# Kernel tuning notes

Measured on AMD Instinct MI355X. Metric: run time of the kernel, lower is better.

The kernel has to match this reference:

```python
import jax, jax.numpy as jnp
import numpy as np

B, T, D, H = 2, 2048, 512, 8
HD = D // H  # head_dim = 64


def setup_inputs() -> dict:
    key = jax.random.key(0)
    k1, k2, k3, k4 = jax.random.split(key, 4)
    scale = 1.0 / np.sqrt(D)
    x = jax.random.normal(k1, (B, T, D), dtype=jnp.float32)
    periods = jax.random.randint(k2, (B, H), 0, 64, dtype=jnp.int32)
    w_qkv = jax.random.normal(k3, (3 * D, D), dtype=jnp.float32) * scale
    b_qkv = jnp.zeros((3 * D,), dtype=jnp.float32)
    w_out = jax.random.normal(k4, (D, D), dtype=jnp.float32) * scale
    b_out = jnp.zeros((D,), dtype=jnp.float32)
    return {"x": x, "periods": periods, "w_qkv": w_qkv, "b_qkv": b_qkv,
            "w_out": w_out, "b_out": b_out}


def reference(x, periods, w_qkv, b_qkv, w_out, b_out):
    # qkv projection: (B,T,3D) -> (3,B,H,T,HD)
    qkv = x @ w_qkv.T + b_qkv
    qkv = qkv.reshape(B, T, 3, H, HD).transpose(2, 0, 3, 1, 4)
    q, k, v = qkv[0], qkv[1], qkv[2]

    # periodic-causal mask: valid iff j <= i and (i-j) % p == 0, p = max(period,1)
    i_idx = jnp.arange(T, dtype=jnp.int32)[:, None]   # (T,1)
    j_idx = jnp.arange(T, dtype=jnp.int32)[None, :]   # (1,T)
    diff = i_idx - j_idx                              # (T,T)
    p = jnp.maximum(periods, 1)[:, :, None, None]     # (B,H,1,1)
    valid = (diff >= 0) & ((diff % p) == 0)           # (B,H,T,T)

    scores = jnp.einsum('bhqd,bhkd->bhqk', q, k) / np.sqrt(HD)
    scores = jnp.where(valid, scores, jnp.finfo(scores.dtype).min)
    attn = jax.nn.softmax(scores, axis=-1)

    out = jnp.einsum('bhqk,bhkd->bhqd', attn, v)
    out = out.transpose(0, 2, 1, 3).reshape(B, T, D)
    return out @ w_out.T + b_out
```

## Files before the change

kernel.cpp:

```cpp
#include <hip/hip_runtime.h>
#include <math.h>

#define B_  2
#define T_  2048
#define D_  512
#define H_  8
#define HD_ 64
#define QKVS (3*D_)

typedef __bf16 bf16x8 __attribute__((ext_vector_type(8)));
typedef float  f32x4  __attribute__((ext_vector_type(4)));

__device__ inline unsigned short f2bf(float f) {
  unsigned int u = __float_as_uint(f);
  return (unsigned short)((u + 0x7FFFu + ((u >> 16) & 1u)) >> 16);
}
__device__ inline unsigned int pack2bf(float lo, float hi) {
  return (unsigned int)f2bf(lo) | ((unsigned int)f2bf(hi) << 16);
}

__global__ void cast_f32_bf16(const float* __restrict__ src,
                              unsigned short* __restrict__ dst, int n4) {
  int i = blockIdx.x * blockDim.x + threadIdx.x;
  if (i < n4) {
    float4 v = ((const float4*)src)[i];
    ushort4 o;
    o.x = f2bf(v.x); o.y = f2bf(v.y); o.z = f2bf(v.z); o.w = f2bf(v.w);
    ((ushort4*)dst)[i] = o;
  }
}

template<int BF16OUT>
__global__ __launch_bounds__(256)
void gemm_nt_mfma(const unsigned short* __restrict__ A,
                  const unsigned short* __restrict__ Bw,
                  const float* __restrict__ bias, void* __restrict__ Cv,
                  int M, int N, int K) {
  __shared__ short Asd[128 * 32];
  __shared__ short Bsd[64 * 32];

  const int tid = threadIdx.x;
  const int w   = tid >> 6;
  const int l   = tid & 63;
  const int wr  = w >> 1;
  const int wc  = w & 1;
  const int q   = l >> 4;
  const int ml  = l & 15;
  const int arow = l >> 2;
  const int kch  = (l & 3) * 8;

  const int rowbase = blockIdx.y * 128;
  const int colbase = blockIdx.x * 64;

  f32x4 acc[4][2] = {};

  for (int k0 = 0; k0 < K; k0 += 32) {
    __syncthreads();
    #pragma unroll
    for (int s = 0; s < 2; ++s) {
      const unsigned short* g =
          A + (size_t)(rowbase + s * 64 + w * 16 + arow) * K + k0 + kch;
      short* lp = &Asd[s * 2048 + w * 512];
      __builtin_amdgcn_global_load_lds(
          (const __attribute__((address_space(1))) void*)g,
          (__attribute__((address_space(3))) void*)lp, 16, 0, 0);
    }
    {
      const unsigned short* g =
          Bw + (size_t)(colbase + w * 16 + arow) * K + k0 + kch;
      short* lp = &Bsd[w * 512];
      __builtin_amdgcn_global_load_lds(
          (const __attribute__((address_space(1))) void*)g,
          (__attribute__((address_space(3))) void*)lp, 16, 0, 0);
    }
    __syncthreads();

    bf16x8 af[4], bfr[2];
    #pragma unroll
    for (int mi = 0; mi < 4; ++mi)
      af[mi] = *(const bf16x8*)&Asd[(wr * 64 + mi * 16 + ml) * 32 + q * 8];
    #pragma unroll
    for (int ni = 0; ni < 2; ++ni)
      bfr[ni] = *(const bf16x8*)&Bsd[(wc * 32 + ni * 16 + ml) * 32 + q * 8];
    #pragma unroll
    for (int mi = 0; mi < 4; ++mi)
      #pragma unroll
      for (int ni = 0; ni < 2; ++ni)
        acc[mi][ni] = __builtin_amdgcn_mfma_f32_16x16x32_bf16(
            af[mi], bfr[ni], acc[mi][ni], 0, 0, 0);
  }

  #pragma unroll
  for (int mi = 0; mi < 4; ++mi) {
    #pragma unroll
    for (int ni = 0; ni < 2; ++ni) {
      const int col = colbase + wc * 32 + ni * 16 + ml;
      const float bv = bias[col];
      #pragma unroll
      for (int r = 0; r < 4; ++r) {
        const int row = rowbase + wr * 64 + mi * 16 + q * 4 + r;
        const float val = acc[mi][ni][r] + bv;
        if (BF16OUT)
          ((unsigned short*)Cv)[(size_t)row * N + col] = f2bf(val);
        else
          ((float*)Cv)[(size_t)row * N + col] = val;
      }
    }
  }
}

template<int BF16OUT>
__global__ __launch_bounds__(256)
void gemm_nt_mfma128(const unsigned short* __restrict__ A,
                     const unsigned short* __restrict__ Bw,
                     const float* __restrict__ bias, void* __restrict__ Cv,
                     int M, int N, int K) {
  __shared__ short Asd[128 * 32];
  __shared__ short Bsd[128 * 32];

  const int tid = threadIdx.x;
  const int w   = tid >> 6;
  const int l   = tid & 63;
  const int wr  = w >> 1;
  const int wc  = w & 1;
  const int q   = l >> 4;
  const int ml  = l & 15;
  const int arow = l >> 2;
  const int kch  = (l & 3) * 8;

  const int rowbase = blockIdx.y * 128;
  const int colbase = blockIdx.x * 128;

  f32x4 acc[4][4] = {};

  for (int k0 = 0; k0 < K; k0 += 32) {
    __syncthreads();
    #pragma unroll
    for (int s = 0; s < 2; ++s) {
      const unsigned short* ga =
          A + (size_t)(rowbase + s * 64 + w * 16 + arow) * K + k0 + kch;
      __builtin_amdgcn_global_load_lds(
          (const __attribute__((address_space(1))) void*)ga,
          (__attribute__((address_space(3))) void*)&Asd[s * 2048 + w * 512],
          16, 0, 0);
      const unsigned short* gb =
          Bw + (size_t)(colbase + s * 64 + w * 16 + arow) * K + k0 + kch;
      __builtin_amdgcn_global_load_lds(
          (const __attribute__((address_space(1))) void*)gb,
          (__attribute__((address_space(3))) void*)&Bsd[s * 2048 + w * 512],
          16, 0, 0);
    }
    __syncthreads();

    bf16x8 af[4], bfr[4];
    #pragma unroll
    for (int mi = 0; mi < 4; ++mi)
      af[mi] = *(const bf16x8*)&Asd[(wr * 64 + mi * 16 + ml) * 32 + q * 8];
    #pragma unroll
    for (int ni = 0; ni < 4; ++ni)
      bfr[ni] = *(const bf16x8*)&Bsd[(wc * 64 + ni * 16 + ml) * 32 + q * 8];
    #pragma unroll
    for (int mi = 0; mi < 4; ++mi)
      #pragma unroll
      for (int ni = 0; ni < 4; ++ni)
        acc[mi][ni] = __builtin_amdgcn_mfma_f32_16x16x32_bf16(
            af[mi], bfr[ni], acc[mi][ni], 0, 0, 0);
  }

  #pragma unroll
  for (int mi = 0; mi < 4; ++mi) {
    #pragma unroll
    for (int ni = 0; ni < 4; ++ni) {
      const int col = colbase + wc * 64 + ni * 16 + ml;
      const float bv = bias[col];
      #pragma unroll
      for (int r = 0; r < 4; ++r) {
        const int row = rowbase + wr * 64 + mi * 16 + q * 4 + r;
        const float val = acc[mi][ni][r] + bv;
        if (BF16OUT)
          ((unsigned short*)Cv)[(size_t)row * N + col] = f2bf(val);
        else
          ((float*)Cv)[(size_t)row * N + col] = val;
      }
    }
  }
}

__global__ __launch_bounds__(64)
void attn_flash(const unsigned short* __restrict__ qkv,
                const int* __restrict__ periods,
                unsigned short* __restrict__ ao) {
  const int bh = blockIdx.x, slot = blockIdx.y;
  int p = periods[bh]; if (p < 1) p = 1;
  const int qt = slot / p;
  const int r  = slot - qt * p;
  const int L  = (T_ - 1 - r) / p + 1;
  if (qt >= ((L + 15) >> 4)) return;
  const int b = bh >> 3, h = bh & 7;
  const int q0 = qt << 4;
  const int nq = min(16, L - q0);
  const int Nk = min(L, q0 + 16);

  const int lane = threadIdx.x;
  const int Q = lane >> 4, c = lane & 15;

  __shared__ unsigned short Qs[16 * 72];
  __shared__ unsigned short Ks[32 * 72];
  __shared__ unsigned short Vs[32 * 70];

  const size_t rowb = (size_t)b * T_ * QKVS + (size_t)h * HD_;

  {
    const int u = lane >> 2, ch3 = lane & 3;
    const int t = q0 + min(u, nq - 1);
    const unsigned short* g = qkv + rowb + (size_t)(r + t * p) * QKVS + ch3 * 16;
    int4 v0 = ((const int4*)g)[0];
    int4 v1 = ((const int4*)g)[1];
    *(int4*)&Qs[u * 72 + ch3 * 16 + 0] = v0;
    *(int4*)&Qs[u * 72 + ch3 * 16 + 8] = v1;
  }
  __syncthreads();
  bf16x8 qf[2];
  qf[0] = *(const bf16x8*)&Qs[c * 72 + Q * 8];
  qf[1] = *(const bf16x8*)&Qs[c * 72 + Q * 8 + 32];

  float m_run = -3.0e38f, l_run = 0.f;
  f32x4 o[4] = {};
  const size_t kb = rowb + D_;
  const size_t vb = rowb + 2 * D_;
  const int kap = lane >> 1, ke = lane & 1;

  for (int k0 = 0; k0 < Nk; k0 += 32) {
    {
      const int t = min(k0 + kap, Nk - 1);
      const unsigned short* gk = qkv + kb + (size_t)(r + t * p) * QKVS + ke * 32;
      const unsigned short* gv = qkv + vb + (size_t)(r + t * p) * QKVS + ke * 32;
      int4 a0 = ((const int4*)gk)[0], a1 = ((const int4*)gk)[1],
           a2 = ((const int4*)gk)[2], a3 = ((const int4*)gk)[3];
      int4 b0 = ((const int4*)gv)[0], b1 = ((const int4*)gv)[1],
           b2 = ((const int4*)gv)[2], b3 = ((const int4*)gv)[3];
      __syncthreads();
      *(int4*)&Ks[kap * 72 + ke * 32 + 0]  = a0;
      *(int4*)&Ks[kap * 72 + ke * 32 + 8]  = a1;
      *(int4*)&Ks[kap * 72 + ke * 32 + 16] = a2;
      *(int4*)&Ks[kap * 72 + ke * 32 + 24] = a3;
      unsigned int* vw = (unsigned int*)Vs + kap * 35 + ke * 16;
      int4 bb[4] = {b0, b1, b2, b3};
      #pragma unroll
      for (int i = 0; i < 4; ++i) {
        vw[i * 4 + 0] = bb[i].x; vw[i * 4 + 1] = bb[i].y;
        vw[i * 4 + 2] = bb[i].z; vw[i * 4 + 3] = bb[i].w;
      }
      __syncthreads();
    }

    f32x4 s[2];
    #pragma unroll
    for (int mt = 0; mt < 2; ++mt) {
      bf16x8 a0 = *(const bf16x8*)&Ks[(mt * 16 + c) * 72 + Q * 8];
      bf16x8 a1 = *(const bf16x8*)&Ks[(mt * 16 + c) * 72 + Q * 8 + 32];
      f32x4 acc = {};
      acc = __builtin_amdgcn_mfma_f32_16x16x32_bf16(a0, qf[0], acc, 0, 0, 0);
      acc = __builtin_amdgcn_mfma_f32_16x16x32_bf16(a1, qf[1], acc, 0, 0, 0);
      s[mt] = acc;
    }

    float pvv[8];
    float tmax = -3.0e38f;
    #pragma unroll
    for (int mt = 0; mt < 2; ++mt)
      #pragma unroll
      for (int rg = 0; rg < 4; ++rg) {
        const int kk = k0 + mt * 16 + Q * 4 + rg;
        float v = s[mt][rg] * 0.125f;
        v = (kk <= q0 + c) ? v : -3.0e38f;
        pvv[mt * 4 + rg] = v;
        tmax = fmaxf(tmax, v);
      }
    tmax = fmaxf(tmax, __shfl_xor(tmax, 16));
    tmax = fmaxf(tmax, __shfl_xor(tmax, 32));
    const float m_new = fmaxf(m_run, tmax);
    const float alpha = __expf(m_run - m_new);
    float tsum = 0.f;
    #pragma unroll
    for (int i = 0; i < 8; ++i) { pvv[i] = __expf(pvv[i] - m_new); tsum += pvv[i]; }
    tsum += __shfl_xor(tsum, 16);
    tsum += __shfl_xor(tsum, 32);
    l_run = l_run * alpha + tsum;
    m_run = m_new;

    unsigned int pk0[2], pk1[2];
    pk0[0] = pack2bf(pvv[0], pvv[1]); pk0[1] = pack2bf(pvv[2], pvv[3]);
    pk1[0] = pack2bf(pvv[4], pvv[5]); pk1[1] = pack2bf(pvv[6], pvv[7]);
    int dw[4];
    const int sq2 = (Q & 1) << 1;
    #pragma unroll
    for (int d = 0; d < 4; ++d) {
      const int src = ((sq2 + (d >> 1)) << 4) + c;
      const int v0 = __shfl((int)pk0[d & 1], src);
      const int v1 = __shfl((int)pk1[d & 1], src);
      dw[d] = (Q >= 2) ? v1 : v0;
    }
    int4 bi = make_int4(dw[0], dw[1], dw[2], dw[3]);
    bf16x8 pb = *(bf16x8*)&bi;

    #pragma unroll
    for (int ch = 0; ch < 4; ++ch) {
      unsigned short vh[8];
      #pragma unroll
      for (int j = 0; j < 8; ++j)
        vh[j] = Vs[(Q * 8 + j) * 70 + ch * 16 + c];
      unsigned int vi[4];
      #pragma unroll
      for (int j = 0; j < 4; ++j)
        vi[j] = (unsigned int)vh[2 * j] | ((unsigned int)vh[2 * j + 1] << 16);
      int4 ai4 = make_int4((int)vi[0], (int)vi[1], (int)vi[2], (int)vi[3]);
      bf16x8 af = *(bf16x8*)&ai4;
      f32x4 oo = o[ch];
      #pragma unroll
      for (int t2 = 0; t2 < 4; ++t2) oo[t2] *= alpha;
      o[ch] = __builtin_amdgcn_mfma_f32_16x16x32_bf16(af, pb, oo, 0, 0, 0);
    }
  }

  if (c < nq) {
    const float invl = 1.f / l_run;
    const int gq = r + (q0 + c) * p;
    unsigned int* dst =
        (unsigned int*)(ao + (size_t)(b * T_ + gq) * D_ + h * HD_);
    #pragma unroll
    for (int ch = 0; ch < 4; ++ch)
      #pragma unroll
      for (int rp = 0; rp < 2; ++rp) {
        const int dhalf = ch * 16 + Q * 4 + rp * 2;
        dst[dhalf >> 1] =
            pack2bf(o[ch][rp * 2] * invl, o[ch][rp * 2 + 1] * invl);
      }
  }
}

extern "C" void kernel_launch(void* const* d_in, const int* in_sizes, int n_in,
                              void* d_out, int out_size, void* d_ws, size_t ws_size,
                              hipStream_t stream) {
  const float* x      = (const float*)d_in[0];
  const int*   period = (const int*)  d_in[1];
  const float* w_qkv  = (const float*)d_in[2];
  const float* b_qkv  = (const float*)d_in[3];
  const float* w_out  = (const float*)d_in[4];
  const float* b_out  = (const float*)d_in[5];
  float* out = (float*)d_out;

  const int M = B_ * T_;

  char* ws = (char*)d_ws;
  unsigned short* xb   = (unsigned short*)(ws);
  unsigned short* wqb  = (unsigned short*)(ws + (size_t)M * D_ * 2);
  unsigned short* wob  = (unsigned short*)(ws + (size_t)M * D_ * 2
                                              + (size_t)QKVS * D_ * 2);
  unsigned short* qkvb = (unsigned short*)(ws + (size_t)M * D_ * 2
                                              + (size_t)QKVS * D_ * 2
                                              + (size_t)D_ * D_ * 2);
  unsigned short* aob  = xb;

  cast_f32_bf16<<<dim3((M * D_ / 4 + 255) / 256), dim3(256), 0, stream>>>(
      x, xb, M * D_ / 4);
  cast_f32_bf16<<<dim3((QKVS * D_ / 4 + 255) / 256), dim3(256), 0, stream>>>(
      w_qkv, wqb, QKVS * D_ / 4);
  cast_f32_bf16<<<dim3((D_ * D_ / 4 + 255) / 256), dim3(256), 0, stream>>>(
      w_out, wob, D_ * D_ / 4);

  gemm_nt_mfma128<1><<<dim3(QKVS / 128, M / 128), dim3(256), 0, stream>>>(
      xb, wqb, b_qkv, qkvb, M, QKVS, D_);

  attn_flash<<<dim3(16, 192), dim3(64), 0, stream>>>(qkvb, period, aob);

  gemm_nt_mfma<0><<<dim3(D_ / 64, M / 128), dim3(256), 0, stream>>>(
      aob, wob, b_out, out, M, D_, D_);
}
```

Before: 125.6 us.

## Share K/V tiles across four waves in attention and fuse cast kernels

The attention kernel now uses 256-thread blocks of four waves. Each wave owns 16 queries of a 64-query group, and all four share one K tile and one transposed V tile in LDS. V is stored transposed, so the PV MFMA operand becomes a single vector LDS read instead of eight scalar gathers plus packing. Waves skip key tiles beyond their causal range, which reduces global K/V traffic per query and shrinks the grid from 192 to 63 slots. The three f32-to-bf16 cast launches are merged into one kernel to save launch overhead, at the cost of idle waves and barrier stalls for the early-query waves in each group.

```diff
diff --git a/kernel.cpp b/kernel.cpp
--- a/kernel.cpp
+++ b/kernel.cpp
@@ -19,15 +19,25 @@
   return (unsigned int)f2bf(lo) | ((unsigned int)f2bf(hi) << 16);
 }
 
-__global__ void cast_f32_bf16(const float* __restrict__ src,
-                              unsigned short* __restrict__ dst, int n4) {
+__global__ void cast_all(const float* __restrict__ x,
+                         const float* __restrict__ wq,
+                         const float* __restrict__ wo,
+                         unsigned short* __restrict__ xb,
+                         unsigned short* __restrict__ wqb,
+                         unsigned short* __restrict__ wob) {
+  const int n_x  = (B_ * T_ * D_) / 4;
+  const int n_wq = (QKVS * D_) / 4;
+  const int n_wo = (D_ * D_) / 4;
   int i = blockIdx.x * blockDim.x + threadIdx.x;
-  if (i < n4) {
-    float4 v = ((const float4*)src)[i];
-    ushort4 o;
-    o.x = f2bf(v.x); o.y = f2bf(v.y); o.z = f2bf(v.z); o.w = f2bf(v.w);
-    ((ushort4*)dst)[i] = o;
-  }
+  const float* src; unsigned short* dst; int off;
+  if (i < n_x)                { src = x;  dst = xb;  off = i; }
+  else if (i < n_x + n_wq)    { src = wq; dst = wqb; off = i - n_x; }
+  else if (i < n_x + n_wq + n_wo) { src = wo; dst = wob; off = i - n_x - n_wq; }
+  else return;
+  float4 v = ((const float4*)src)[off];
+  ushort4 o;
+  o.x = f2bf(v.x); o.y = f2bf(v.y); o.z = f2bf(v.z); o.w = f2bf(v.w);
+  ((ushort4*)dst)[off] = o;
 }
 
 template<int BF16OUT>
@@ -186,148 +196,142 @@
   }
 }
 
-__global__ __launch_bounds__(64)
-void attn_flash(const unsigned short* __restrict__ qkv,
-                const int* __restrict__ periods,
-                unsigned short* __restrict__ ao) {
+__global__ __launch_bounds__(256)
+void attn_flash2(const unsigned short* __restrict__ qkv,
+                 const int* __restrict__ periods,
+                 unsigned short* __restrict__ ao) {
   const int bh = blockIdx.x, slot = blockIdx.y;
   int p = periods[bh]; if (p < 1) p = 1;
-  const int qt = slot / p;
-  const int r  = slot - qt * p;
+  const int g  = slot / p;
+  const int r  = slot - g * p;
   const int L  = (T_ - 1 - r) / p + 1;
-  if (qt >= ((L + 15) >> 4)) return;
+  const int q0 = g << 6;
+  if (q0 >= L) return;
   const int b = bh >> 3, h = bh & 7;
-  const int q0 = qt << 4;
-  const int nq = min(16, L - q0);
-  const int Nk = min(L, q0 + 16);
-
-  const int lane = threadIdx.x;
+  const int Lrem = L - q0;
+  const int Nkb  = min(L, q0 + 64);
+
+  const int tid  = threadIdx.x;
+  const int w    = tid >> 6;
+  const int lane = tid & 63;
   const int Q = lane >> 4, c = lane & 15;
 
-  __shared__ unsigned short Qs[16 * 72];
-  __shared__ unsigned short Ks[32 * 72];
-  __shared__ unsigned short Vs[32 * 70];
+  __shared__ __align__(16) unsigned short Qs[64 * 72];
+  __shared__ __align__(16) unsigned short Ks[32 * 72];
+  __shared__ __align__(16) unsigned short Vt[64 * 40];
 
   const size_t rowb = (size_t)b * T_ * QKVS + (size_t)h * HD_;
 
   {
-    const int u = lane >> 2, ch3 = lane & 3;
-    const int t = q0 + min(u, nq - 1);
-    const unsigned short* g = qkv + rowb + (size_t)(r + t * p) * QKVS + ch3 * 16;
-    int4 v0 = ((const int4*)g)[0];
-    int4 v1 = ((const int4*)g)[1];
-    *(int4*)&Qs[u * 72 + ch3 * 16 + 0] = v0;
-    *(int4*)&Qs[u * 72 + ch3 * 16 + 8] = v1;
+    const int u = tid >> 2, ch4 = (tid & 3) * 16;
+    const int t = q0 + min(u, Lrem - 1);
+    const unsigned short* gq = qkv + rowb + (size_t)(r + t * p) * QKVS + ch4;
+    int4 v0 = ((const int4*)gq)[0];
+    int4 v1 = ((const int4*)gq)[1];
+    *(int4*)&Qs[u * 72 + ch4 + 0] = v0;
+    *(int4*)&Qs[u * 72 + ch4 + 8] = v1;
   }
   __syncthreads();
   bf16x8 qf[2];
-  qf[0] = *(const bf16x8*)&Qs[c * 72 + Q * 8];
-  qf[1] = *(const bf16x8*)&Qs[c * 72 + Q * 8 + 32];
+  qf[0] = *(const bf16x8*)&Qs[(w * 16 + c) * 72 + Q * 8];
+  qf[1] = *(const bf16x8*)&Qs[(w * 16 + c) * 72 + Q * 8 + 32];
+
+  const int qb      = w * 16;
+  const int nqw     = min(16, Lrem - qb);
+  const int qglob   = q0 + qb + c;
+  const int mylastk = q0 + qb + 15;
 
   float m_run = -3.0e38f, l_run = 0.f;
   f32x4 o[4] = {};
   const size_t kb = rowb + D_;
   const size_t vb = rowb + 2 * D_;
-  const int kap = lane >> 1, ke = lane & 1;
-
-  for (int k0 = 0; k0 < Nk; k0 += 32) {
+
+  const int krow = tid >> 3, koff = (tid & 7) * 8;
+  const int vkey = tid & 31, vd0 = (tid >> 5) * 8;
+
+  for (int k0 = 0; k0 < Nkb; k0 += 32) {
     {
-      const int t = min(k0 + kap, Nk - 1);
-      const unsigned short* gk = qkv + kb + (size_t)(r + t * p) * QKVS + ke * 32;
-      const unsigned short* gv = qkv + vb + (size_t)(r + t * p) * QKVS + ke * 32;
-      int4 a0 = ((const int4*)gk)[0], a1 = ((const int4*)gk)[1],
-           a2 = ((const int4*)gk)[2], a3 = ((const int4*)gk)[3];
-      int4 b0 = ((const int4*)gv)[0], b1 = ((const int4*)gv)[1],
-           b2 = ((const int4*)gv)[2], b3 = ((const int4*)gv)[3];
+      const int tk = min(k0 + krow, Nkb - 1);
+      const int tv = min(k0 + vkey, Nkb - 1);
+      int4 kv = *(const int4*)(qkv + kb + (size_t)(r + tk * p) * QKVS + koff);
+      int4 vv = *(const int4*)(qkv + vb + (size_t)(r + tv * p) * QKVS + vd0);
+      unsigned short vh[8];
+      *(int4*)vh = vv;
       __syncthreads();
-      *(int4*)&Ks[kap * 72 + ke * 32 + 0]  = a0;
-      *(int4*)&Ks[kap * 72 + ke * 32 + 8]  = a1;
-      *(int4*)&Ks[kap * 72 + ke * 32 + 16] = a2;
-      *(int4*)&Ks[kap * 72 + ke * 32 + 24] = a3;
-      unsigned int* vw = (unsigned int*)Vs + kap * 35 + ke * 16;
-      int4 bb[4] = {b0, b1, b2, b3};
-      #pragma unroll
-      for (int i = 0; i < 4; ++i) {
-        vw[i * 4 + 0] = bb[i].x; vw[i * 4 + 1] = bb[i].y;
-        vw[i * 4 + 2] = bb[i].z; vw[i * 4 + 3] = bb[i].w;
-      }
+      *(int4*)&Ks[krow * 72 + koff] = kv;
+      #pragma unroll
+      for (int j = 0; j < 8; ++j)
+        Vt[(vd0 + j) * 40 + vkey] = vh[j];
       __syncthreads();
     }
 
-    f32x4 s[2];
-    #pragma unroll
-    for (int mt = 0; mt < 2; ++mt) {
-      bf16x8 a0 = *(const bf16x8*)&Ks[(mt * 16 + c) * 72 + Q * 8];
-      bf16x8 a1 = *(const bf16x8*)&Ks[(mt * 16 + c) * 72 + Q * 8 + 32];
-      f32x4 acc = {};
-      acc = __builtin_amdgcn_mfma_f32_16x16x32_bf16(a0, qf[0], acc, 0, 0, 0);
-      acc = __builtin_amdgcn_mfma_f32_16x16x32_bf16(a1, qf[1], acc, 0, 0, 0);
-      s[mt] = acc;
-    }
-
-    float pvv[8];
-    float tmax = -3.0e38f;
-    #pragma unroll
-    for (int mt = 0; mt < 2; ++mt)
-      #pragma unroll
-      for (int rg = 0; rg < 4; ++rg) {
-        const int kk = k0 + mt * 16 + Q * 4 + rg;
-        float v = s[mt][rg] * 0.125f;
-        v = (kk <= q0 + c) ? v : -3.0e38f;
-        pvv[mt * 4 + rg] = v;
-        tmax = fmaxf(tmax, v);
-      }
-    tmax = fmaxf(tmax, __shfl_xor(tmax, 16));
-    tmax = fmaxf(tmax, __shfl_xor(tmax, 32));
-    const float m_new = fmaxf(m_run, tmax);
-    const float alpha = __expf(m_run - m_new);
-    float tsum = 0.f;
-    #pragma unroll
-    for (int i = 0; i < 8; ++i) { pvv[i] = __expf(pvv[i] - m_new); tsum += pvv[i]; }
-    tsum += __shfl_xor(tsum, 16);
-    tsum += __shfl_xor(tsum, 32);
-    l_run = l_run * alpha + tsum;
-    m_run = m_new;
-
-    unsigned int pk0[2], pk1[2];
-    pk0[0] = pack2bf(pvv[0], pvv[1]); pk0[1] = pack2bf(pvv[2], pvv[3]);
-    pk1[0] = pack2bf(pvv[4], pvv[5]); pk1[1] = pack2bf(pvv[6], pvv[7]);
-    int dw[4];
-    const int sq2 = (Q & 1) << 1;
-    #pragma unroll
-    for (int d = 0; d < 4; ++d) {
-      const int src = ((sq2 + (d >> 1)) << 4) + c;
-      const int v0 = __shfl((int)pk0[d & 1], src);
-      const int v1 = __shfl((int)pk1[d & 1], src);
-      dw[d] = (Q >= 2) ? v1 : v0;
-    }
-    int4 bi = make_int4(dw[0], dw[1], dw[2], dw[3]);
-    bf16x8 pb = *(bf16x8*)&bi;
-
-    #pragma unroll
-    for (int ch = 0; ch < 4; ++ch) {
-      unsigned short vh[8];
-      #pragma unroll
-      for (int j = 0; j < 8; ++j)
-        vh[j] = Vs[(Q * 8 + j) * 70 + ch * 16 + c];
-      unsigned int vi[4];
-      #pragma unroll
-      for (int j = 0; j < 4; ++j)
-        vi[j] = (unsigned int)vh[2 * j] | ((unsigned int)vh[2 * j + 1] << 16);
-      int4 ai4 = make_int4((int)vi[0], (int)vi[1], (int)vi[2], (int)vi[3]);
-      bf16x8 af = *(bf16x8*)&ai4;
-      f32x4 oo = o[ch];
-      #pragma unroll
-      for (int t2 = 0; t2 < 4; ++t2) oo[t2] *= alpha;
-      o[ch] = __builtin_amdgcn_mfma_f32_16x16x32_bf16(af, pb, oo, 0, 0, 0);
-    }
-  }
-
-  if (c < nq) {
+    if (nqw > 0 && k0 <= mylastk) {
+      f32x4 s[2];
+      #pragma unroll
+      for (int mt = 0; mt < 2; ++mt) {
+        bf16x8 a0 = *(const bf16x8*)&Ks[(mt * 16 + c) * 72 + Q * 8];
+        bf16x8 a1 = *(const bf16x8*)&Ks[(mt * 16 + c) * 72 + Q * 8 + 32];
+        f32x4 acc = {};
+        acc = __builtin_amdgcn_mfma_f32_16x16x32_bf16(a0, qf[0], acc, 0, 0, 0);
+        acc = __builtin_amdgcn_mfma_f32_16x16x32_bf16(a1, qf[1], acc, 0, 0, 0);
+        s[mt] = acc;
+      }
+
+      float pvv[8];
+      float tmax = -3.0e38f;
+      #pragma unroll
+      for (int mt = 0; mt < 2; ++mt)
+        #pragma unroll
+        for (int rg = 0; rg < 4; ++rg) {
+          const int kk = k0 + mt * 16 + Q * 4 + rg;
+          float v = s[mt][rg] * 0.125f;
+          v = (kk <= qglob) ? v : -3.0e38f;
+          pvv[mt * 4 + rg] = v;
+          tmax = fmaxf(tmax, v);
+        }
+      tmax = fmaxf(tmax, __shfl_xor(tmax, 16));
+      tmax = fmaxf(tmax, __shfl_xor(tmax, 32));
+      const float m_new = fmaxf(m_run, tmax);
+      const float alpha = __expf(m_run - m_new);
+      float tsum = 0.f;
+      #pragma unroll
+      for (int i = 0; i < 8; ++i) { pvv[i] = __expf(pvv[i] - m_new); tsum += pvv[i]; }
+      tsum += __shfl_xor(tsum, 16);
+      tsum += __shfl_xor(tsum, 32);
+      l_run = l_run * alpha + tsum;
+      m_run = m_new;
+
+      unsigned int pk0[2], pk1[2];
+      pk0[0] = pack2bf(pvv[0], pvv[1]); pk0[1] = pack2bf(pvv[2], pvv[3]);
+      pk1[0] = pack2bf(pvv[4], pvv[5]); pk1[1] = pack2bf(pvv[6], pvv[7]);
+      int dw[4];
+      const int sq2 = (Q & 1) << 1;
+      #pragma unroll
+      for (int d = 0; d < 4; ++d) {
+        const int src = ((sq2 + (d >> 1)) << 4) + c;
+        const int v0 = __shfl((int)pk0[d & 1], src);
+        const int v1 = __shfl((int)pk1[d & 1], src);
+        dw[d] = (Q >= 2) ? v1 : v0;
+      }
+      int4 bi = make_int4(dw[0], dw[1], dw[2], dw[3]);
+      bf16x8 pb = *(bf16x8*)&bi;
+
+      #pragma unroll
+      for (int ch = 0; ch < 4; ++ch) {
+        bf16x8 af = *(const bf16x8*)&Vt[(ch * 16 + c) * 40 + Q * 8];
+        f32x4 oo = o[ch];
+        #pragma unroll
+        for (int t2 = 0; t2 < 4; ++t2) oo[t2] *= alpha;
+        o[ch] = __builtin_amdgcn_mfma_f32_16x16x32_bf16(af, pb, oo, 0, 0, 0);
+      }
+    }
+  }
+
+  if (nqw > 0 && c < nqw) {
     const float invl = 1.f / l_run;
-    const int gq = r + (q0 + c) * p;
+    const int tok = r + (q0 + qb + c) * p;
     unsigned int* dst =
-        (unsigned int*)(ao + (size_t)(b * T_ + gq) * D_ + h * HD_);
+        (unsigned int*)(ao + (size_t)(b * T_ + tok) * D_ + h * HD_);
     #pragma unroll
     for (int ch = 0; ch < 4; ++ch)
       #pragma unroll
@@ -362,17 +366,16 @@
                                               + (size_t)D_ * D_ * 2);
   unsigned short* aob  = xb;
 
-  cast_f32_bf16<<<dim3((M * D_ / 4 + 255) / 256), dim3(256), 0, stream>>>(
-      x, xb, M * D_ / 4);
-  cast_f32_bf16<<<dim3((QKVS * D_ / 4 + 255) / 256), dim3(256), 0, stream>>>(
-      w_qkv, wqb, QKVS * D_ / 4);
-  cast_f32_bf16<<<dim3((D_ * D_ / 4 + 255) / 256), dim3(256), 0, stream>>>(
-      w_out, wob, D_ * D_ / 4);
+  {
+    const int n4 = (M * D_ + QKVS * D_ + D_ * D_) / 4;
+    cast_all<<<dim3((n4 + 255) / 256), dim3(256), 0, stream>>>(
+        x, w_qkv, w_out, xb, wqb, wob);
+  }
 
   gemm_nt_mfma128<1><<<dim3(QKVS / 128, M / 128), dim3(256), 0, stream>>>(
       xb, wqb, b_qkv, qkvb, M, QKVS, D_);
 
-  attn_flash<<<dim3(16, 192), dim3(64), 0, stream>>>(qkvb, period, aob);
+  attn_flash2<<<dim3(16, 63), dim3(256), 0, stream>>>(qkvb, period, aob);
 
   gemm_nt_mfma<0><<<dim3(D_ / 64, M / 128), dim3(256), 0, stream>>>(
       aob, wob, b_out, out, M, D_, D_);
```

Result: faster. 116.6 us (-7.1%).
